# Performance work log

Measured on AMD Instinct MI355X. Metric: run time of the kernel, lower is better.

## Reference

```python
import jax, jax.numpy as jnp
import numpy as np

T = 524288
INPUT_LEN = 64
N_MEMORY = 64
OUTPUT_LEN = 32


def setup_inputs() -> dict:
    key = jax.random.key(0)
    k_x, k_w1, k_b1, k_w2, k_b2 = jax.random.split(key, 5)
    s = 0.05  # tf.random_normal_initializer default stddev
    return {
        "inputs": jax.random.normal(k_x, (T, INPUT_LEN), dtype=jnp.float32),
        "W1": s * jax.random.normal(k_w1, (INPUT_LEN, 2 * N_MEMORY), dtype=jnp.float32),
        "B1": s * jax.random.normal(k_b1, (1, 2 * N_MEMORY), dtype=jnp.float32),
        "W2": s * jax.random.normal(k_w2, (N_MEMORY, OUTPUT_LEN), dtype=jnp.float32),
        "B2": s * jax.random.normal(k_b2, (1, OUTPUT_LEN), dtype=jnp.float32),
    }


def reference(inputs, W1, B1, W2, B2):
    n_memory = W2.shape[0]
    # gates: h = sigmoid(x W1 + B1), split into left/right halves  [T, M] each
    h = jax.nn.sigmoid(inputs @ W1 + B1)
    left, right = jnp.split(h, 2, axis=1)
    prod = left * right
    # affine linear recurrence: u_t = prod_{t-1} * u_{t-1} + (1 - left_{t-1}), u_0 = 0
    a = prod[:-1]            # [T-1, M] multiplicative coeffs
    b = 1.0 - left[:-1]      # [T-1, M] additive terms

    def step(u, ab):
        a_t, b_t = ab
        u = a_t * u + b_t
        return u, u

    u0 = jnp.zeros((n_memory,), dtype=inputs.dtype)
    _, us = jax.lax.scan(step, u0, (a, b))
    z = jnp.concatenate([u0[None, :], us], axis=0)  # [T, M]
    out = z @ W2 + B2                               # [T, output_len]
    return out
```

## Files before the change

### kernel.cpp

```cpp
#include <hip/hip_runtime.h>

#define TT    524288
#define CHUNK 512
#define NCH   (TT / CHUNK)
#define SUB   64
#define NSUB  (CHUNK / SUB)

typedef __attribute__((ext_vector_type(8))) short short8;
typedef __attribute__((ext_vector_type(4))) float f32x4;

__device__ __forceinline__ unsigned short f2bf(float f) {
    union { float f; unsigned u; } v; v.f = f;
    unsigned r = v.u + 0x7FFFu + ((v.u >> 16) & 1u);
    return (unsigned short)(r >> 16);
}
__device__ __forceinline__ float sigf(float v) {
    return 1.0f / (1.0f + __expf(-v));
}

template <bool EMIT>
__global__ __launch_bounds__(256, 2)
void dphase(const float* __restrict__ x, const float* __restrict__ W1,
            const float* __restrict__ B1, const float* __restrict__ W2,
            const float* __restrict__ B2, const float* __restrict__ carry,
            float* __restrict__ Aout, float* __restrict__ Bout,
            float* __restrict__ out)
{
    __shared__ __align__(16) short  W1t[128 * 72];
    __shared__ float  B1s[128];
    __shared__ __align__(16) short  Xs[SUB * 72];
    __shared__ __align__(16) float2 abf[SUB * 66];
    __shared__ float  segA[4 * 66], segB[4 * 66];
    __shared__ float  ucur[64];
    __shared__ __align__(16) short  W2t[32 * 72];
    __shared__ float  B2s[32];
    __shared__ __align__(16) short  Zs[SUB * 72];

    const int tid  = threadIdx.x;
    const int c    = blockIdx.x;
    const int wave = tid >> 6;
    const int lane = tid & 63;
    const int quad = lane >> 4;
    const int lr   = lane & 15;

    for (int i = tid; i < 2048; i += 256) {
        float4 w4 = ((const float4*)W1)[i];
        int k = i >> 5, n0 = (i & 31) * 4;
        W1t[(n0 + 0) * 72 + k] = (short)f2bf(w4.x);
        W1t[(n0 + 1) * 72 + k] = (short)f2bf(w4.y);
        W1t[(n0 + 2) * 72 + k] = (short)f2bf(w4.z);
        W1t[(n0 + 3) * 72 + k] = (short)f2bf(w4.w);
    }
    if (tid < 128) B1s[tid] = B1[tid];
    if (EMIT) {
        for (int i = tid; i < 512; i += 256) {
            float4 w4 = ((const float4*)W2)[i];
            int k = i >> 3, n0 = (i & 7) * 4;
            W2t[(n0 + 0) * 72 + k] = (short)f2bf(w4.x);
            W2t[(n0 + 1) * 72 + k] = (short)f2bf(w4.y);
            W2t[(n0 + 2) * 72 + k] = (short)f2bf(w4.z);
            W2t[(n0 + 3) * 72 + k] = (short)f2bf(w4.w);
        }
        if (tid < 32) B2s[tid] = B2[tid];
        if (tid < 64) ucur[tid] = carry[c * 64 + tid];
    }

    const float4* xg = (const float4*)(x + (size_t)c * CHUNK * 64);
    float4 xr0 = xg[tid], xr1 = xg[tid + 256], xr2 = xg[tid + 512], xr3 = xg[tid + 768];

    float sA = 1.0f, sB = 0.0f;

    for (int s = 0; s < NSUB; ++s) {
        {
            float4 v; int f;
#define PUTX(R, J) { v = (R); f = tid + 256 * (J); int row = f >> 4, c4 = (f & 15) * 4; \
            unsigned lo = (unsigned)f2bf(v.x) | ((unsigned)f2bf(v.y) << 16); \
            unsigned hi = (unsigned)f2bf(v.z) | ((unsigned)f2bf(v.w) << 16); \
            *(uint2*)&Xs[row * 72 + c4] = make_uint2(lo, hi); }
            PUTX(xr0, 0) PUTX(xr1, 1) PUTX(xr2, 2) PUTX(xr3, 3)
#undef PUTX
        }
        __syncthreads();

        if (s + 1 < NSUB) {
            const float4* xn = xg + (size_t)(s + 1) * 1024;
            xr0 = xn[tid]; xr1 = xn[tid + 256]; xr2 = xn[tid + 512]; xr3 = xn[tid + 768];
        }

        f32x4 acc[8];
        #pragma unroll
        for (int j = 0; j < 8; ++j) {
            float b = B1s[j * 16 + lr];
            acc[j][0] = b; acc[j][1] = b; acc[j][2] = b; acc[j][3] = b;
        }
        const short8 a0 = *(const short8*)&Xs[(wave * 16 + lr) * 72 + quad * 8];
        const short8 a1 = *(const short8*)&Xs[(wave * 16 + lr) * 72 + quad * 8 + 32];
        #pragma unroll
        for (int j = 0; j < 8; ++j) {
            const short8 b0 = *(const short8*)&W1t[(j * 16 + lr) * 72 + quad * 8];
            const short8 b1 = *(const short8*)&W1t[(j * 16 + lr) * 72 + quad * 8 + 32];
            acc[j] = __builtin_amdgcn_mfma_f32_16x16x32_bf16(a0, b0, acc[j], 0, 0, 0);
            acc[j] = __builtin_amdgcn_mfma_f32_16x16x32_bf16(a1, b1, acc[j], 0, 0, 0);
        }

        #pragma unroll
        for (int j = 0; j < 4; ++j) {
            #pragma unroll
            for (int r = 0; r < 4; ++r) {
                float hl = sigf(acc[j][r]);
                float hr = sigf(acc[j + 4][r]);
                int m = wave * 16 + quad * 4 + r;
                abf[m * 66 + j * 16 + lr] = make_float2(hl * hr, 1.0f - hl);
            }
        }
        __syncthreads();

        float A = 1.0f, Bv = 0.0f;
        #pragma unroll
        for (int t = 0; t < 16; ++t) {
            float2 f2 = abf[(wave * 16 + t) * 66 + lane];
            Bv = fmaf(f2.x, Bv, f2.y); A *= f2.x;
        }
        segA[wave * 66 + lane] = A;
        segB[wave * 66 + lane] = Bv;
        __syncthreads();

        if (EMIT) {
            float u = ucur[lane];
            #pragma unroll
            for (int q = 0; q < 3; ++q)
                if (q < wave) u = fmaf(segA[q * 66 + lane], u, segB[q * 66 + lane]);
            #pragma unroll
            for (int t = 0; t < 16; ++t) {
                float2 f2 = abf[(wave * 16 + t) * 66 + lane];
                Zs[(wave * 16 + t) * 72 + lane] = (short)f2bf(u);
                u = fmaf(f2.x, u, f2.y);
            }
            const float unew = u;
            __syncthreads();
            if (wave == 3) ucur[lane] = unew;

            const short8 za0 = *(const short8*)&Zs[(wave * 16 + lr) * 72 + quad * 8];
            const short8 za1 = *(const short8*)&Zs[(wave * 16 + lr) * 72 + quad * 8 + 32];
            const size_t row0g = (size_t)c * CHUNK + (size_t)s * SUB;
            #pragma unroll
            for (int nt = 0; nt < 2; ++nt) {
                f32x4 cc;
                float b = B2s[nt * 16 + lr];
                cc[0] = b; cc[1] = b; cc[2] = b; cc[3] = b;
                const short8 b0 = *(const short8*)&W2t[(nt * 16 + lr) * 72 + quad * 8];
                const short8 b1 = *(const short8*)&W2t[(nt * 16 + lr) * 72 + quad * 8 + 32];
                cc = __builtin_amdgcn_mfma_f32_16x16x32_bf16(za0, b0, cc, 0, 0, 0);
                cc = __builtin_amdgcn_mfma_f32_16x16x32_bf16(za1, b1, cc, 0, 0, 0);
                #pragma unroll
                for (int r = 0; r < 4; ++r) {
                    int m = wave * 16 + quad * 4 + r;
                    out[(row0g + m) * 32 + nt * 16 + lr] = cc[r];
                }
            }
        } else {
            if (tid < 64) {
                #pragma unroll
                for (int q = 0; q < 4; ++q) {
                    float A2 = segA[q * 66 + tid], B2v = segB[q * 66 + tid];
                    sB = fmaf(A2, sB, B2v); sA *= A2;
                }
            }
        }
    }

    if (!EMIT && tid < 64) { Aout[c * 64 + tid] = sA; Bout[c * 64 + tid] = sB; }
}

__global__ void carry_scan(const float* __restrict__ Aar, const float* __restrict__ Bar,
                           float* __restrict__ carry)
{
    __shared__ float sA[8 * 66], sB[8 * 66];
    const int tid = threadIdx.x;
    const int ch = tid & 63, seg = tid >> 6;
    const int c0 = seg * (NCH / 8);

    float A = 1.0f, B = 0.0f;
    #pragma unroll 8
    for (int i = 0; i < NCH / 8; ++i) {
        const int idx = c0 + i;
        const float a = Aar[idx * 64 + ch];
        const float b = Bar[idx * 64 + ch];
        B = fmaf(a, B, b); A *= a;
    }
    sA[seg * 66 + ch] = A;
    sB[seg * 66 + ch] = B;
    __syncthreads();

    float u = 0.0f;
    #pragma unroll
    for (int q = 0; q < 7; ++q)
        if (q < seg) u = fmaf(sA[q * 66 + ch], u, sB[q * 66 + ch]);
    #pragma unroll 8
    for (int i = 0; i < NCH / 8; ++i) {
        const int idx = c0 + i;
        carry[idx * 64 + ch] = u;
        u = fmaf(Aar[idx * 64 + ch], u, Bar[idx * 64 + ch]);
    }
}

extern "C" void kernel_launch(void* const* d_in, const int* in_sizes, int n_in,
                              void* d_out, int out_size, void* d_ws, size_t ws_size,
                              hipStream_t stream)
{
    const float* x  = (const float*)d_in[0];
    const float* W1 = (const float*)d_in[1];
    const float* B1 = (const float*)d_in[2];
    const float* W2 = (const float*)d_in[3];
    const float* B2 = (const float*)d_in[4];
    float* out = (float*)d_out;

    float* Aar   = (float*)d_ws;
    float* Bar   = Aar + NCH * 64;
    float* carry = Bar + NCH * 64;

    dphase<false><<<NCH, 256, 0, stream>>>(x, W1, B1, W2, B2, nullptr,
                                           Aar, Bar, nullptr);
    carry_scan<<<1, 512, 0, stream>>>(Aar, Bar, carry);
    dphase<true><<<NCH, 256, 0, stream>>>(x, W1, B1, W2, B2, carry,
                                          nullptr, nullptr, out);
}
```

Before: 328.1 us.

## Shrink LDS with packed bf16 gates, alias X/Z buffer, widen carry scan

Gate coefficients a,b are now packed as two bf16 values in one 32-bit word instead of a float2, and the X and Z staging buffers share one LDS array. Together these cut LDS use so occupancy can rise to 3 blocks per CU. The sigmoid uses a hardware reciprocal, one barrier in the emit path is moved, and the carry scan runs on 1024 threads with 16 segments. The bf16 gate storage lowers precision in the 512-step recurrence, which can compound error. The aliased buffer relies on barrier ordering between the Z writes and the next sub-block's X writes.

Measured after the change: 301.5 us. 1.09x faster.

```diff
diff --git a/kernel.cpp b/kernel.cpp
--- a/kernel.cpp
+++ b/kernel.cpp
@@ -14,27 +14,37 @@
     unsigned r = v.u + 0x7FFFu + ((v.u >> 16) & 1u);
     return (unsigned short)(r >> 16);
 }
+__device__ __forceinline__ unsigned packbf2(float a, float b) {
+    union { float f; unsigned u; } va, vb; va.f = a; vb.f = b;
+    unsigned ra = va.u + 0x7FFFu + ((va.u >> 16) & 1u);
+    unsigned rb = vb.u + 0x7FFFu + ((vb.u >> 16) & 1u);
+    return (ra >> 16) | (rb & 0xFFFF0000u);
+}
+__device__ __forceinline__ float2 unpackbf2(unsigned w) {
+    union { unsigned u; float f; } a, b;
+    a.u = w << 16; b.u = w & 0xFFFF0000u;
+    return make_float2(a.f, b.f);
+}
 __device__ __forceinline__ float sigf(float v) {
-    return 1.0f / (1.0f + __expf(-v));
+    return __builtin_amdgcn_rcpf(1.0f + __expf(-v));
 }
 
 template <bool EMIT>
-__global__ __launch_bounds__(256, 2)
+__global__ __launch_bounds__(256, 3)
 void dphase(const float* __restrict__ x, const float* __restrict__ W1,
             const float* __restrict__ B1, const float* __restrict__ W2,
             const float* __restrict__ B2, const float* __restrict__ carry,
             float* __restrict__ Aout, float* __restrict__ Bout,
             float* __restrict__ out)
 {
-    __shared__ __align__(16) short  W1t[128 * 72];
-    __shared__ float  B1s[128];
-    __shared__ __align__(16) short  Xs[SUB * 72];
-    __shared__ __align__(16) float2 abf[SUB * 66];
-    __shared__ float  segA[4 * 66], segB[4 * 66];
-    __shared__ float  ucur[64];
-    __shared__ __align__(16) short  W2t[32 * 72];
-    __shared__ float  B2s[32];
-    __shared__ __align__(16) short  Zs[SUB * 72];
+    __shared__ __align__(16) short    W1t[128 * 72];
+    __shared__ float    B1s[128];
+    __shared__ __align__(16) short    XZ[SUB * 72];
+    __shared__ unsigned abp[SUB * 65];
+    __shared__ float    segA[4 * 66], segB[4 * 66];
+    __shared__ float    ucur[64];
+    __shared__ __align__(16) short    W2t[32 * 72];
+    __shared__ float    B2s[32];
 
     const int tid  = threadIdx.x;
     const int c    = blockIdx.x;
@@ -76,7 +86,7 @@
 #define PUTX(R, J) { v = (R); f = tid + 256 * (J); int row = f >> 4, c4 = (f & 15) * 4; \
             unsigned lo = (unsigned)f2bf(v.x) | ((unsigned)f2bf(v.y) << 16); \
             unsigned hi = (unsigned)f2bf(v.z) | ((unsigned)f2bf(v.w) << 16); \
-            *(uint2*)&Xs[row * 72 + c4] = make_uint2(lo, hi); }
+            *(uint2*)&XZ[row * 72 + c4] = make_uint2(lo, hi); }
             PUTX(xr0, 0) PUTX(xr1, 1) PUTX(xr2, 2) PUTX(xr3, 3)
 #undef PUTX
         }
@@ -93,8 +103,8 @@
             float b = B1s[j * 16 + lr];
             acc[j][0] = b; acc[j][1] = b; acc[j][2] = b; acc[j][3] = b;
         }
-        const short8 a0 = *(const short8*)&Xs[(wave * 16 + lr) * 72 + quad * 8];
-        const short8 a1 = *(const short8*)&Xs[(wave * 16 + lr) * 72 + quad * 8 + 32];
+        const short8 a0 = *(const short8*)&XZ[(wave * 16 + lr) * 72 + quad * 8];
+        const short8 a1 = *(const short8*)&XZ[(wave * 16 + lr) * 72 + quad * 8 + 32];
         #pragma unroll
         for (int j = 0; j < 8; ++j) {
             const short8 b0 = *(const short8*)&W1t[(j * 16 + lr) * 72 + quad * 8];
@@ -110,7 +120,7 @@
                 float hl = sigf(acc[j][r]);
                 float hr = sigf(acc[j + 4][r]);
                 int m = wave * 16 + quad * 4 + r;
-                abf[m * 66 + j * 16 + lr] = make_float2(hl * hr, 1.0f - hl);
+                abp[m * 65 + j * 16 + lr] = packbf2(hl * hr, 1.0f - hl);
             }
         }
         __syncthreads();
@@ -118,7 +128,7 @@
         float A = 1.0f, Bv = 0.0f;
         #pragma unroll
         for (int t = 0; t < 16; ++t) {
-            float2 f2 = abf[(wave * 16 + t) * 66 + lane];
+            float2 f2 = unpackbf2(abp[(wave * 16 + t) * 65 + lane]);
             Bv = fmaf(f2.x, Bv, f2.y); A *= f2.x;
         }
         segA[wave * 66 + lane] = A;
@@ -132,16 +142,14 @@
                 if (q < wave) u = fmaf(segA[q * 66 + lane], u, segB[q * 66 + lane]);
             #pragma unroll
             for (int t = 0; t < 16; ++t) {
-                float2 f2 = abf[(wave * 16 + t) * 66 + lane];
-                Zs[(wave * 16 + t) * 72 + lane] = (short)f2bf(u);
+                float2 f2 = unpackbf2(abp[(wave * 16 + t) * 65 + lane]);
+                XZ[(wave * 16 + t) * 72 + lane] = (short)f2bf(u);
                 u = fmaf(f2.x, u, f2.y);
             }
-            const float unew = u;
-            __syncthreads();
-            if (wave == 3) ucur[lane] = unew;
-
-            const short8 za0 = *(const short8*)&Zs[(wave * 16 + lr) * 72 + quad * 8];
-            const short8 za1 = *(const short8*)&Zs[(wave * 16 + lr) * 72 + quad * 8 + 32];
+            if (wave == 3) ucur[lane] = u;
+
+            const short8 za0 = *(const short8*)&XZ[(wave * 16 + lr) * 72 + quad * 8];
+            const short8 za1 = *(const short8*)&XZ[(wave * 16 + lr) * 72 + quad * 8 + 32];
             const size_t row0g = (size_t)c * CHUNK + (size_t)s * SUB;
             #pragma unroll
             for (int nt = 0; nt < 2; ++nt) {
@@ -158,6 +166,7 @@
                     out[(row0g + m) * 32 + nt * 16 + lr] = cc[r];
                 }
             }
+            __syncthreads();
         } else {
             if (tid < 64) {
                 #pragma unroll
@@ -175,14 +184,14 @@
 __global__ void carry_scan(const float* __restrict__ Aar, const float* __restrict__ Bar,
                            float* __restrict__ carry)
 {
-    __shared__ float sA[8 * 66], sB[8 * 66];
+    __shared__ float sA[16 * 66], sB[16 * 66];
     const int tid = threadIdx.x;
     const int ch = tid & 63, seg = tid >> 6;
-    const int c0 = seg * (NCH / 8);
+    const int c0 = seg * (NCH / 16);
 
     float A = 1.0f, B = 0.0f;
     #pragma unroll 8
-    for (int i = 0; i < NCH / 8; ++i) {
+    for (int i = 0; i < NCH / 16; ++i) {
         const int idx = c0 + i;
         const float a = Aar[idx * 64 + ch];
         const float b = Bar[idx * 64 + ch];
@@ -194,10 +203,10 @@
 
     float u = 0.0f;
     #pragma unroll
-    for (int q = 0; q < 7; ++q)
+    for (int q = 0; q < 15; ++q)
         if (q < seg) u = fmaf(sA[q * 66 + ch], u, sB[q * 66 + ch]);
     #pragma unroll 8
-    for (int i = 0; i < NCH / 8; ++i) {
+    for (int i = 0; i < NCH / 16; ++i) {
         const int idx = c0 + i;
         carry[idx * 64 + ch] = u;
         u = fmaf(Aar[idx * 64 + ch], u, Bar[idx * 64 + ch]);
@@ -221,7 +230,7 @@
 
     dphase<false><<<NCH, 256, 0, stream>>>(x, W1, B1, W2, B2, nullptr,
                                            Aar, Bar, nullptr);
-    carry_scan<<<1, 512, 0, stream>>>(Aar, Bar, carry);
+    carry_scan<<<1, 1024, 0, stream>>>(Aar, Bar, carry);
     dphase<true><<<NCH, 256, 0, stream>>>(x, W1, B1, W2, B2, carry,
                                           nullptr, nullptr, out);
 }
```
